# Optimization experiments

Measured on AMD Instinct MI355X. Metric: run time of the kernel, lower is better.

## Reference

```python
import jax, jax.numpy as jnp
import numpy as np
from jax import lax

PADDING_L = 30  # causal: kernel_size - 1


def setup_inputs() -> dict:
    key = jax.random.key(0)
    k1, k2 = jax.random.split(key)
    T, B, C = 4096, 8, 1024
    H, K = 16, 31
    x = jax.random.normal(k1, (T, B, C), dtype=jnp.float32)
    weight = jax.random.normal(k2, (H, K), dtype=jnp.float32)
    return {"x": x, "weight": weight}


def reference(x, weight):
    # x: [T, B, C]; weight: [H, K]
    T, B, C = x.shape
    H, K = weight.shape
    R = C // H  # channels per head share the same kernel
    # weight_softmax=True: normalize kernel taps per head
    w = jax.nn.softmax(weight, axis=-1)            # [H, K]
    wc = jnp.repeat(w, R, axis=0)[:, None, :]      # [C, 1, K] depthwise kernel
    xb = jnp.transpose(x, (1, 2, 0))               # [B, C, T]
    # lightconv_cuda: out[b,c,t] = sum_k w[h(c),k] * x_pad[b,c,t+k],
    # left pad = padding_l, right pad = K-1-padding_l (cross-correlation)
    out = lax.conv_general_dilated(
        xb, wc,
        window_strides=(1,),
        padding=[(PADDING_L, K - 1 - PADDING_L)],
        feature_group_count=C,
        dimension_numbers=("NCH", "OIH", "NCH"),
    )                                              # [B, C, T]
    return jnp.transpose(out, (2, 0, 1))           # [T, B, C]
```

## Files before the change

### kernel.cpp

```cpp
#include <hip/hip_runtime.h>
#include <math.h>

#define T_DIM 4096
#define B_DIM 8
#define C_DIM 1024
#define H_DIM 16
#define K_DIM 31
#define NT 32
#define L_SEG 128
#define BLOCK 256
#define DP 8
#define STRIDE (B_DIM * C_DIM)


template <int M>
__device__ __forceinline__ void warm(const float* pw,
                                     float (&xr)[DP],
                                     const float (&tp)[NT],
                                     float (&acc)[NT]) {
    if constexpr (M < 31) {
        const float v = xr[(M + 1) & 7];
        #pragma unroll
        for (int j = 1; j <= 30; ++j) {
            if (j >= 31 - M)
                acc[(M + 1 + j) & 31] = fmaf(tp[31 - j], v, acc[(M + 1 + j) & 31]);
        }
        xr[(M + 1) & 7] = pw[(long)(M + DP) * STRIDE];
        warm<M + 1>(pw, xr, tp, acc);
    }
}

template <int SB, bool LAST>
__device__ __forceinline__ void bstep(const float* pin,
                                      float* pout,
                                      float (&xr)[DP],
                                      const float (&tp)[NT],
                                      float (&acc)[NT]) {
    if constexpr (SB < 32) {
        const float v = xr[SB & 7];
        pout[(long)SB * STRIDE] = fmaf(tp[31], v, acc[SB]);
        #pragma unroll
        for (int j = 1; j <= 30; ++j)
            acc[(SB + j) & 31] = fmaf(tp[31 - j], v, acc[(SB + j) & 31]);
        acc[(SB + 31) & 31] = 0.0f;
        if constexpr (!LAST || SB < 24)
            xr[SB & 7] = pin[(long)(SB + DP) * STRIDE];
        bstep<SB + 1, LAST>(pin, pout, xr, tp, acc);
    }
}

__global__ __launch_bounds__(BLOCK, 4) void lightconv_kernel(
    const float* __restrict__ x,
    const float* __restrict__ w,
    float* __restrict__ out)
{
    const int tid    = threadIdx.x;
    const int wv     = tid >> 6;
    const int colBlk = blockIdx.x;
    const int tseg   = blockIdx.y;
    const int cc     = colBlk * BLOCK + tid;
    const long t0    = (long)tseg * L_SEG;

    float tp[NT];
    {
        const float* wr = w + (((colBlk & 3) << 2) + wv) * K_DIM;
        float tv[K_DIM];
        float m = -1e30f;
        #pragma unroll
        for (int k = 0; k < K_DIM; ++k) { tv[k] = wr[k]; m = fmaxf(m, tv[k]); }
        float s = 0.f;
        #pragma unroll
        for (int k = 0; k < K_DIM; ++k) { tv[k] = __expf(tv[k] - m); s += tv[k]; }
        const float inv = 1.0f / s;
        tp[0] = 0.0f;
        #pragma unroll
        for (int k = 0; k < K_DIM; ++k)
            tp[k + 1] = __int_as_float(__builtin_amdgcn_readfirstlane(
                            __float_as_int(tv[k] * inv)));
    }

    float acc[NT];
    #pragma unroll
    for (int i = 0; i < NT; ++i) acc[i] = 0.0f;

    float xr[DP];
    if (tseg > 0) {
        const float* pw = x + (t0 - 31) * STRIDE + cc;
        #pragma unroll
        for (int m = 0; m < DP; ++m)
            xr[(m + 1) & 7] = pw[(long)m * STRIDE];
        warm<0>(pw, xr, tp, acc);
    } else {
        #pragma unroll
        for (int m = 0; m < DP; ++m)
            xr[m] = x[(long)m * STRIDE + cc];
    }

    const float* pin = x   + t0 * STRIDE + cc;
    float*       pout = out + t0 * STRIDE + cc;
    #pragma unroll 1
    for (int b = 0; b < 3; ++b) {
        bstep<0, false>(pin, pout, xr, tp, acc);
        pin  += 32 * STRIDE;
        pout += 32 * STRIDE;
    }
    bstep<0, true>(pin, pout, xr, tp, acc);
}

extern "C" void kernel_launch(void* const* d_in, const int* in_sizes, int n_in,
                              void* d_out, int out_size, void* d_ws, size_t ws_size,
                              hipStream_t stream) {
    const float* x = (const float*)d_in[0];
    const float* w = (const float*)d_in[1];
    float* out = (float*)d_out;

    dim3 grid((B_DIM * C_DIM) / BLOCK, T_DIM / L_SEG);
    lightconv_kernel<<<grid, BLOCK, 0, stream>>>(x, w, out);
}
```

Baseline: 244.2 us.

## Process two adjacent channels per thread with float2 loads and deeper prefetch

Each thread now handles two adjacent channels using 2-wide float vectors for loads, stores and accumulators. The grid is halved, the input prefetch ring grows from 8 to 16 entries, and launch bounds drop to 2 blocks per CU. The aim is fewer, wider memory transactions and a chance to use packed FMAs. In exchange, the softmaxed taps can no longer be made wave-uniform with readfirstlane, because each wave now spans two heads. That raises VGPR pressure and halves the number of waves available to hide latency.

```diff
diff --git a/kernel.cpp b/kernel.cpp
--- a/kernel.cpp
+++ b/kernel.cpp
@@ -9,23 +9,27 @@
 #define NT 32
 #define L_SEG 128
 #define BLOCK 256
-#define DP 8
+#define DP 16
 #define STRIDE (B_DIM * C_DIM)
+
+typedef __attribute__((ext_vector_type(2))) float f32x2;
 
 
 template <int M>
 __device__ __forceinline__ void warm(const float* pw,
-                                     float (&xr)[DP],
+                                     f32x2 (&xr)[DP],
                                      const float (&tp)[NT],
-                                     float (&acc)[NT]) {
+                                     f32x2 (&acc)[NT]) {
     if constexpr (M < 31) {
-        const float v = xr[(M + 1) & 7];
+        const f32x2 v = xr[(M + 1) & 15];
         #pragma unroll
         for (int j = 1; j <= 30; ++j) {
-            if (j >= 31 - M)
-                acc[(M + 1 + j) & 31] = fmaf(tp[31 - j], v, acc[(M + 1 + j) & 31]);
+            if (j >= 31 - M) {
+                acc[(M + 1 + j) & 31].x = fmaf(tp[31 - j], v.x, acc[(M + 1 + j) & 31].x);
+                acc[(M + 1 + j) & 31].y = fmaf(tp[31 - j], v.y, acc[(M + 1 + j) & 31].y);
+            }
         }
-        xr[(M + 1) & 7] = pw[(long)(M + DP) * STRIDE];
+        xr[(M + 1) & 15] = *(const f32x2*)(pw + (long)(M + DP) * STRIDE);
         warm<M + 1>(pw, xr, tp, acc);
     }
 }
@@ -33,37 +37,43 @@
 template <int SB, bool LAST>
 __device__ __forceinline__ void bstep(const float* pin,
                                       float* pout,
-                                      float (&xr)[DP],
+                                      f32x2 (&xr)[DP],
                                       const float (&tp)[NT],
-                                      float (&acc)[NT]) {
+                                      f32x2 (&acc)[NT]) {
     if constexpr (SB < 32) {
-        const float v = xr[SB & 7];
-        pout[(long)SB * STRIDE] = fmaf(tp[31], v, acc[SB]);
+        const f32x2 v = xr[SB & 15];
+        f32x2 o;
+        o.x = fmaf(tp[31], v.x, acc[SB].x);
+        o.y = fmaf(tp[31], v.y, acc[SB].y);
+        *(f32x2*)(pout + (long)SB * STRIDE) = o;
         #pragma unroll
-        for (int j = 1; j <= 30; ++j)
-            acc[(SB + j) & 31] = fmaf(tp[31 - j], v, acc[(SB + j) & 31]);
-        acc[(SB + 31) & 31] = 0.0f;
-        if constexpr (!LAST || SB < 24)
-            xr[SB & 7] = pin[(long)(SB + DP) * STRIDE];
+        for (int j = 1; j <= 30; ++j) {
+            acc[(SB + j) & 31].x = fmaf(tp[31 - j], v.x, acc[(SB + j) & 31].x);
+            acc[(SB + j) & 31].y = fmaf(tp[31 - j], v.y, acc[(SB + j) & 31].y);
+        }
+        acc[(SB + 31) & 31].x = 0.0f;
+        acc[(SB + 31) & 31].y = 0.0f;
+        if constexpr (!LAST || SB < 32 - DP)
+            xr[SB & 15] = *(const f32x2*)(pin + (long)(SB + DP) * STRIDE);
         bstep<SB + 1, LAST>(pin, pout, xr, tp, acc);
     }
 }
 
-__global__ __launch_bounds__(BLOCK, 4) void lightconv_kernel(
+__global__ __launch_bounds__(BLOCK, 2) void lightconv_kernel(
     const float* __restrict__ x,
     const float* __restrict__ w,
     float* __restrict__ out)
 {
     const int tid    = threadIdx.x;
-    const int wv     = tid >> 6;
     const int colBlk = blockIdx.x;
     const int tseg   = blockIdx.y;
-    const int cc     = colBlk * BLOCK + tid;
+    const int col0   = (colBlk * BLOCK + tid) * 2;
     const long t0    = (long)tseg * L_SEG;
 
     float tp[NT];
     {
-        const float* wr = w + (((colBlk & 3) << 2) + wv) * K_DIM;
+        const int head = (col0 >> 6) & 15;
+        const float* wr = w + head * K_DIM;
         float tv[K_DIM];
         float m = -1e30f;
         #pragma unroll
@@ -74,30 +84,28 @@
         const float inv = 1.0f / s;
         tp[0] = 0.0f;
         #pragma unroll
-        for (int k = 0; k < K_DIM; ++k)
-            tp[k + 1] = __int_as_float(__builtin_amdgcn_readfirstlane(
-                            __float_as_int(tv[k] * inv)));
+        for (int k = 0; k < K_DIM; ++k) tp[k + 1] = tv[k] * inv;
     }
 
-    float acc[NT];
+    f32x2 acc[NT];
     #pragma unroll
-    for (int i = 0; i < NT; ++i) acc[i] = 0.0f;
+    for (int i = 0; i < NT; ++i) { acc[i].x = 0.0f; acc[i].y = 0.0f; }
 
-    float xr[DP];
+    f32x2 xr[DP];
     if (tseg > 0) {
-        const float* pw = x + (t0 - 31) * STRIDE + cc;
+        const float* pw = x + (t0 - 31) * STRIDE + col0;
         #pragma unroll
         for (int m = 0; m < DP; ++m)
-            xr[(m + 1) & 7] = pw[(long)m * STRIDE];
+            xr[(m + 1) & 15] = *(const f32x2*)(pw + (long)m * STRIDE);
         warm<0>(pw, xr, tp, acc);
     } else {
         #pragma unroll
         for (int m = 0; m < DP; ++m)
-            xr[m] = x[(long)m * STRIDE + cc];
+            xr[m] = *(const f32x2*)(x + (long)m * STRIDE + col0);
     }
 
-    const float* pin = x   + t0 * STRIDE + cc;
-    float*       pout = out + t0 * STRIDE + cc;
+    const float* pin  = x   + t0 * STRIDE + col0;
+    float*       pout = out + t0 * STRIDE + col0;
     #pragma unroll 1
     for (int b = 0; b < 3; ++b) {
         bstep<0, false>(pin, pout, xr, tp, acc);
@@ -114,6 +122,6 @@
     const float* w = (const float*)d_in[1];
     float* out = (float*)d_out;
 
-    dim3 grid((B_DIM * C_DIM) / BLOCK, T_DIM / L_SEG);
+    dim3 grid((B_DIM * C_DIM) / (BLOCK * 2), T_DIM / L_SEG);
     lightconv_kernel<<<grid, BLOCK, 0, stream>>>(x, w, out);
 }
```

Result: faster. 238.0 us (-2.5%).
